# Kernel tuning notes

Measured on AMD Instinct MI355X. Metric: run time of the kernel, lower is better.

Reference implementation:

```python
import jax, jax.numpy as jnp
import numpy as np

TEMPERATURE = 0.07
MARGIN = 0.15
HARD_NEG_RATIO = 0.5


def setup_inputs() -> dict:
    key = jax.random.key(0)
    k1, k2, k3 = jax.random.split(key, 3)
    B, D = 4096, 128
    drug_emb = jax.random.normal(k1, (B, D), dtype=jnp.float32)
    se_emb = jax.random.normal(k2, (B, D), dtype=jnp.float32)
    # labels spread over [0, 5) so that |diff| > 1.0 negatives exist
    labels = jax.random.uniform(k3, (B,), dtype=jnp.float32) * 5.0
    return {"drug_emb": drug_emb, "se_emb": se_emb, "labels": labels}


def _single_branch_loss(z, labels):
    B = z.shape[0]
    # F.normalize(z, dim=-1): divide by norm clamped to eps
    z = z / jnp.maximum(jnp.linalg.norm(z, axis=-1, keepdims=True), 1e-12)
    sim = jnp.matmul(z, z.T) / TEMPERATURE                      # [B, B]
    label_diff = jnp.abs(labels[None, :] - labels[:, None])     # [B, B]
    self_mask = ~jnp.eye(B, dtype=bool)
    pos_weight = jnp.exp(-label_diff / MARGIN) * self_mask      # soft positives
    neg_mask = (label_diff > 1.0) & self_mask

    # k = max(int(mean per-row negative count * ratio), 1), capped at B-1
    mean_negs = jnp.mean(jnp.sum(neg_mask.astype(jnp.float32), axis=1))
    k = jnp.maximum((mean_negs * HARD_NEG_RATIO).astype(jnp.int32), 1)
    k = jnp.minimum(k, B - 1)

    sim_max = jax.lax.stop_gradient(jnp.max(sim, axis=1, keepdims=True))
    logits = sim - sim_max

    # hard-negative top-k per row, as a static-shape rank test (jit-safe)
    neg_sim = jnp.where(neg_mask, sim, -jnp.inf)
    ranks = jnp.argsort(jnp.argsort(-neg_sim, axis=1), axis=1)  # 0 = largest
    hard_neg_mask = (ranks < k) & neg_mask

    any_neg = jnp.any(neg_mask)
    denom_mask = jnp.where(any_neg, hard_neg_mask | (pos_weight > 0.1), self_mask)

    exp_denom = jnp.sum(jnp.exp(logits) * denom_mask, axis=1, keepdims=True) + 1e-8
    log_prob = logits - jnp.log(exp_denom)
    weighted_log_prob = jnp.sum(pos_weight * log_prob, axis=1)
    denom = jnp.maximum(jnp.sum(pos_weight, axis=1), 1e-8)
    return -jnp.mean(weighted_log_prob / denom)


def reference(drug_emb, se_emb, labels):
    loss_drug = _single_branch_loss(drug_emb, labels)
    loss_se = _single_branch_loss(se_emb, labels)
    loss_cross = _single_branch_loss(drug_emb * se_emb, labels)
    return (loss_drug + loss_se + loss_cross) / 3.0
```

## Files before the change

kernel.cpp:

```cpp
#include <hip/hip_runtime.h>
#include <math.h>

#define BB 4096
#define DD 128
#define KLO 0x3E7FFFFFu
#define KHI 0xC1800000u
#define SH0 19
#define NBALLOC 4352

typedef __attribute__((ext_vector_type(8))) short bf16x8;
typedef __attribute__((ext_vector_type(4))) float f32x4;
typedef __attribute__((ext_vector_type(4))) _Float16 f16x4;

__device__ __forceinline__ unsigned fkey(float x){
    int b = __float_as_int(x);
    return (unsigned)(b ^ ((b >> 31) | 0x80000000));
}
__device__ __forceinline__ float funkey(unsigned u){
    unsigned b = (u & 0x80000000u) ? (u & 0x7fffffffu) : ~u;
    return __uint_as_float(b);
}

__device__ __forceinline__ float blkSumF(float v, volatile float* sh){
    #pragma unroll
    for (int o = 32; o > 0; o >>= 1) v += __shfl_down(v, o);
    int t = threadIdx.x;
    __syncthreads();
    if ((t & 63) == 0) sh[t >> 6] = v;
    __syncthreads();
    return (sh[0] + sh[1]) + (sh[2] + sh[3]);
}
__device__ __forceinline__ int blkSumI(int v, volatile int* sh){
    #pragma unroll
    for (int o = 32; o > 0; o >>= 1) v += __shfl_down(v, o);
    int t = threadIdx.x;
    __syncthreads();
    if ((t & 63) == 0) sh[t >> 6] = v;
    __syncthreads();
    return (sh[0] + sh[1]) + (sh[2] + sh[3]);
}

__global__ void krn_normalize(const float* __restrict__ drug, const float* __restrict__ se,
                              ushort* __restrict__ Z){
    int row = blockIdx.x, br = blockIdx.y, t = threadIdx.x;
    float dv = drug[row * DD + t];
    float sv = se[row * DD + t];
    float v = (br == 0) ? dv : ((br == 1) ? sv : dv * sv);
    float sq = v * v;
    #pragma unroll
    for (int o = 32; o > 0; o >>= 1) sq += __shfl_down(sq, o);
    __shared__ float sh[2];
    if ((t & 63) == 0) sh[t >> 6] = sq;
    __syncthreads();
    float nrm = sqrtf(sh[0] + sh[1]);
    float outv = v / fmaxf(nrm, 1e-12f);
    unsigned u = __float_as_uint(outv);
    unsigned r = (u + 0x7FFFu + ((u >> 16) & 1u)) >> 16;
    int col = t ^ ((row & 7) << 3);
    Z[((size_t)br * BB + row) * DD + col] = (ushort)r;
}

__global__ __launch_bounds__(256) void krn_labelstats(const float* __restrict__ labels,
                                                      int* __restrict__ NC,
                                                      float* __restrict__ PWS,
                                                      int* __restrict__ ntot){
    __shared__ float lab[BB];
    __shared__ int shi[4];
    __shared__ float shf[4];
    int t = threadIdx.x;
    #pragma unroll
    for (int e = 0; e < 4; ++e)
        ((float4*)lab)[t + e * 256] = ((const float4*)labels)[t + e * 256];
    __syncthreads();
    int i0 = blockIdx.x * 16;
    int ctot = 0;
    for (int ii = 0; ii < 16; ++ii){
        float li = lab[i0 + ii];
        int c = 0;
        float pws = 0.f;
        #pragma unroll
        for (int e = 0; e < 16; ++e){
            float d = fabsf(li - lab[t + e * 256]);
            c += (d > 1.0f) ? 1 : 0;
            pws += __expf(d * (-1.0f / 0.15f));
        }
        int C = blkSumI(c, shi);
        float P = blkSumF(pws, shf);
        if (t == 0){
            NC[i0 + ii] = C;
            PWS[i0 + ii] = P - 1.0f;
            ctot += C;
        }
    }
    if (t == 0) atomicAdd(ntot, ctot);
}

__global__ void krn_calck(const int* __restrict__ ntot, int* __restrict__ kflags){
    int N = *ntot;
    int k = N >> 13;
    if (k < 1) k = 1;
    if (k > BB - 1) k = BB - 1;
    kflags[0] = k;
    kflags[1] = (N > 0) ? 1 : 0;
}

__device__ __forceinline__ bf16x8 frag_ld(const ushort* base, int row, int e0){
    int e = e0 ^ ((row & 7) << 3);
    return *(const bf16x8*)(base + row * DD + e);
}

__global__ __launch_bounds__(256) void krn_gemm(const ushort* __restrict__ Z,
                                                _Float16* __restrict__ sim, size_t simStride,
                                                int r0){
    __shared__ ushort As[128 * DD];
    __shared__ ushort Bs[128 * DD];
    const ushort* Zb = Z + (size_t)blockIdx.z * (BB * DD);
    _Float16* simz = sim + (size_t)blockIdx.z * simStride;
    int t = threadIdx.x;
    int rowbase = r0 + blockIdx.y * 128;
    int colbase = blockIdx.x * 128;

    {
        const float4* gA = (const float4*)(Zb + (size_t)rowbase * DD);
        const float4* gB = (const float4*)(Zb + (size_t)colbase * DD);
        float4* lA = (float4*)As;
        float4* lB = (float4*)Bs;
        #pragma unroll
        for (int it = 0; it < 8; ++it){
            lA[it * 256 + t] = gA[it * 256 + t];
            lB[it * 256 + t] = gB[it * 256 + t];
        }
    }
    __syncthreads();

    int wid = t >> 6, lane = t & 63;
    int wr = (wid >> 1) * 64, wc = (wid & 1) * 64;
    int fr = lane & 15, fq = lane >> 4;

    f32x4 acc[4][4];
    #pragma unroll
    for (int m = 0; m < 4; ++m)
        #pragma unroll
        for (int n = 0; n < 4; ++n)
            acc[m][n] = (f32x4){0.f, 0.f, 0.f, 0.f};

    #pragma unroll
    for (int ks = 0; ks < 4; ++ks){
        int e0 = ks * 32 + fq * 8;
        bf16x8 a0 = frag_ld(As, wr + 0 * 16 + fr, e0);
        bf16x8 a1 = frag_ld(As, wr + 1 * 16 + fr, e0);
        bf16x8 a2 = frag_ld(As, wr + 2 * 16 + fr, e0);
        bf16x8 a3 = frag_ld(As, wr + 3 * 16 + fr, e0);
        bf16x8 b0 = frag_ld(Bs, wc + 0 * 16 + fr, e0);
        bf16x8 b1 = frag_ld(Bs, wc + 1 * 16 + fr, e0);
        bf16x8 b2 = frag_ld(Bs, wc + 2 * 16 + fr, e0);
        bf16x8 b3 = frag_ld(Bs, wc + 3 * 16 + fr, e0);
        acc[0][0] = __builtin_amdgcn_mfma_f32_16x16x32_bf16(a0, b0, acc[0][0], 0, 0, 0);
        acc[0][1] = __builtin_amdgcn_mfma_f32_16x16x32_bf16(a0, b1, acc[0][1], 0, 0, 0);
        acc[0][2] = __builtin_amdgcn_mfma_f32_16x16x32_bf16(a0, b2, acc[0][2], 0, 0, 0);
        acc[0][3] = __builtin_amdgcn_mfma_f32_16x16x32_bf16(a0, b3, acc[0][3], 0, 0, 0);
        acc[1][0] = __builtin_amdgcn_mfma_f32_16x16x32_bf16(a1, b0, acc[1][0], 0, 0, 0);
        acc[1][1] = __builtin_amdgcn_mfma_f32_16x16x32_bf16(a1, b1, acc[1][1], 0, 0, 0);
        acc[1][2] = __builtin_amdgcn_mfma_f32_16x16x32_bf16(a1, b2, acc[1][2], 0, 0, 0);
        acc[1][3] = __builtin_amdgcn_mfma_f32_16x16x32_bf16(a1, b3, acc[1][3], 0, 0, 0);
        acc[2][0] = __builtin_amdgcn_mfma_f32_16x16x32_bf16(a2, b0, acc[2][0], 0, 0, 0);
        acc[2][1] = __builtin_amdgcn_mfma_f32_16x16x32_bf16(a2, b1, acc[2][1], 0, 0, 0);
        acc[2][2] = __builtin_amdgcn_mfma_f32_16x16x32_bf16(a2, b2, acc[2][2], 0, 0, 0);
        acc[2][3] = __builtin_amdgcn_mfma_f32_16x16x32_bf16(a2, b3, acc[2][3], 0, 0, 0);
        acc[3][0] = __builtin_amdgcn_mfma_f32_16x16x32_bf16(a3, b0, acc[3][0], 0, 0, 0);
        acc[3][1] = __builtin_amdgcn_mfma_f32_16x16x32_bf16(a3, b1, acc[3][1], 0, 0, 0);
        acc[3][2] = __builtin_amdgcn_mfma_f32_16x16x32_bf16(a3, b2, acc[3][2], 0, 0, 0);
        acc[3][3] = __builtin_amdgcn_mfma_f32_16x16x32_bf16(a3, b3, acc[3][3], 0, 0, 0);
    }

    const float invT = 1.0f / 0.07f;
    int srow0 = blockIdx.y * 128 + wr + fq * 4;
    int scol0 = colbase + wc + fr;
    #pragma unroll
    for (int m = 0; m < 4; ++m){
        #pragma unroll
        for (int n = 0; n < 4; ++n){
            f32x4 c = acc[m][n];
            #pragma unroll
            for (int j = 0; j < 4; ++j)
                simz[(size_t)(srow0 + m * 16 + j) * BB + scol0 + n * 16] = (_Float16)(c[j] * invT);
        }
    }
}

__global__ __launch_bounds__(256) void krn_stats(const _Float16* __restrict__ sim, size_t simStride,
                                                 const float* __restrict__ labels,
                                                 const int* __restrict__ NC,
                                                 const float* __restrict__ PWSg,
                                                 const int* __restrict__ kflags,
                                                 float* __restrict__ rowloss, int r0){
    __shared__ int hist[NBALLOC];
    __shared__ int wsum[4];
    __shared__ float redm[4], redb[4];
    __shared__ float redf[4];
    __shared__ unsigned selb[3];
    __shared__ unsigned sel2[2];
    __shared__ int cnt;
    __shared__ unsigned list[96];

    int t = threadIdx.x;
    int bi = blockIdx.y;
    int row = blockIdx.x;
    int i = r0 + row;
    float li = labels[i];

    #pragma unroll
    for (int e = 0; e < 17; ++e) hist[t + e * 256] = 0;
    __syncthreads();

    const _Float16* srow = sim + (size_t)bi * simStride + (size_t)row * BB;
    const f16x4* sp = (const f16x4*)srow;
    const float4* lp = (const float4*)labels;

    float s[16];
    unsigned negbits = 0, posbits = 0;
    float m = -INFINITY, psim = 0.f;

    #pragma unroll
    for (int e = 0; e < 4; ++e){
        f16x4 hv = sp[t + e * 256];
        float4 lv = lp[t + e * 256];
        float lc[4] = {lv.x, lv.y, lv.z, lv.w};
        #pragma unroll
        for (int c = 0; c < 4; ++c){
            int idx = e * 4 + c;
            float v = (float)hv[c];
            s[idx] = v;
            m = fmaxf(m, v);
            float d = fabsf(li - lc[c]);
            float pw = __expf(d * (-1.0f / 0.15f));
            psim = fmaf(pw, v, psim);
            if (d > 1.0f){
                negbits |= 1u << idx;
                atomicAdd(&hist[(fkey(v) - KLO) >> SH0], 1);
            } else if (d < 0.34538776f){
                posbits |= 1u << idx;
            }
        }
    }

    #pragma unroll
    for (int o = 32; o > 0; o >>= 1){
        m = fmaxf(m, __shfl_down(m, o));
        psim += __shfl_down(psim, o);
    }
    __syncthreads();
    if ((t & 63) == 0){
        int w = t >> 6;
        redm[w] = m; redb[w] = psim;
    }
    __syncthreads();
    float M    = fmaxf(fmaxf(redm[0], redm[1]), fmaxf(redm[2], redm[3]));
    float PSIM = (redb[0] + redb[1]) + (redb[2] + redb[3]);

    int kk = kflags[0], anyneg = kflags[1];
    int NCv = NC[i];
    int mode = anyneg ? ((NCv <= kk) ? 1 : 0) : 2;

    unsigned ukth = 0;
    int rfin = 0;
    if (mode == 0){
        unsigned klo = KLO, khi = KHI;
        int sh = SH0;
        int rp = kk;
        bool ready = true;
        while (true){
            if (klo == khi){ ukth = klo; rfin = rp; break; }
            if (!ready){
                #pragma unroll
                for (int e = 0; e < 17; ++e) hist[t + e * 256] = 0;
                __syncthreads();
                #pragma unroll
                for (int idx = 0; idx < 16; ++idx){
                    if (negbits & (1u << idx)){
                        unsigned u = fkey(s[idx]);
                        if (u >= klo && u <= khi)
                            atomicAdd(&hist[(u - klo) >> sh], 1);
                    }
                }
                __syncthreads();
            }
            ready = false;
            int g = 255 - t;
            int base = g * 17;
            int ls = 0;
            #pragma unroll
            for (int e = 0; e < 17; ++e) ls += hist[base + e];
            int v = ls;
            #pragma unroll
            for (int o = 1; o < 64; o <<= 1){
                int u2 = __shfl_up(v, o);
                if ((t & 63) >= o) v += u2;
            }
            if ((t & 63) == 63) wsum[t >> 6] = v;
            __syncthreads();
            int w = t >> 6;
            int pre = (w > 0 ? wsum[0] : 0) + (w > 1 ? wsum[1] : 0) + (w > 2 ? wsum[2] : 0);
            v += pre;
            int aec = v - ls;
            if (aec < rp && rp <= v){
                int cum = aec;
                #pragma unroll
                for (int e = 16; e >= 0; --e){
                    int c = hist[base + e];
                    if (cum < rp && rp <= cum + c){
                        selb[0] = (unsigned)(base + e);
                        selb[1] = (unsigned)cum;
                        selb[2] = (unsigned)c;
                        break;
                    }
                    cum += c;
                }
            }
            __syncthreads();
            unsigned B = selb[0];
            int ae = (int)selb[1];
            int c  = (int)selb[2];
            rp -= ae;
            klo += B << sh;
            unsigned nhi = klo + ((1u << sh) - 1u);
            if (nhi < khi) khi = nhi;
            if (c <= 96){
                if (t == 0) cnt = 0;
                __syncthreads();
                #pragma unroll
                for (int idx = 0; idx < 16; ++idx){
                    if (negbits & (1u << idx)){
                        unsigned u = fkey(s[idx]);
                        if (u >= klo && u <= khi){
                            int p = atomicAdd(&cnt, 1);
                            list[p] = u;
                        }
                    }
                }
                __syncthreads();
                int cc = cnt;
                if (t < cc){
                    unsigned kj = list[t];
                    int g2 = 0, e2 = 0;
                    for (int mm = 0; mm < cc; ++mm){
                        unsigned km = list[mm];
                        g2 += (km > kj) ? 1 : 0;
                        e2 += (km == kj) ? 1 : 0;
                    }
                    if (g2 < rp && rp <= g2 + e2){ sel2[0] = kj; sel2[1] = (unsigned)g2; }
                }
                __syncthreads();
                ukth = sel2[0];
                rfin = rp - (int)sel2[1];
                break;
            }
            {
                unsigned range = khi - klo;
                int bits = 32 - __clz(range);
                sh = (bits > 12) ? (bits - 12) : 0;
            }
            __syncthreads();
        }
    }

    float skth = (mode == 0) ? funkey(ukth) : INFINITY;
    unsigned em = (mode == 2) ? 0xFFFFu : ((mode == 1) ? (negbits | posbits) : posbits);
    float El = 0.f;
    #pragma unroll
    for (int idx = 0; idx < 16; ++idx){
        unsigned bit = 1u << idx;
        bool dm = (em & bit) != 0u;
        if (negbits & bit) dm = dm || (s[idx] > skth);
        if (dm) El += __expf(s[idx] - M);
    }
    float Etot = blkSumF(El, redf);

    if (t == 0){
        if (mode == 0) Etot += (float)rfin * __expf(skth - M);
        float s_self = (float)srow[i];
        Etot -= __expf(s_self - M);
        float PWSc  = PWSg[i];
        float PSIMc = PSIM - s_self;
        float logE = __logf(Etot + 1e-8f);
        float wl = (PSIMc - M * PWSc) - PWSc * logE;
        rowloss[bi * BB + i] = wl / fmaxf(PWSc, 1e-8f);
    }
}

__global__ void krn_final(const float* __restrict__ rowloss, float* __restrict__ out){
    __shared__ float redf[4];
    int t = threadIdx.x;
    float total = 0.f;
    for (int b = 0; b < 3; ++b){
        float ssum = 0.f;
        for (int e = 0; e < 16; ++e) ssum += rowloss[b * BB + t + e * 256];
        float S = blkSumF(ssum, redf);
        total += S * (1.0f / BB);
    }
    if (t == 0) out[0] = -total / 3.0f;
}

extern "C" void kernel_launch(void* const* d_in, const int* in_sizes, int n_in,
                              void* d_out, int out_size, void* d_ws, size_t ws_size,
                              hipStream_t stream){
    const float* drug   = (const float*)d_in[0];
    const float* se     = (const float*)d_in[1];
    const float* labels = (const float*)d_in[2];
    float* out = (float*)d_out;
    char* ws = (char*)d_ws;

    const size_t zbytes = (size_t)3 * BB * DD * sizeof(ushort);
    const size_t tail   = (size_t)(3 + 1 + 1) * BB * sizeof(float) + 256;

    int slab = BB;
    while (slab > 128 && zbytes + tail + (size_t)3 * slab * BB * sizeof(_Float16) > ws_size)
        slab >>= 1;
    size_t simStride = (size_t)slab * BB;

    ushort* Z          = (ushort*)ws;
    _Float16* simbuf   = (_Float16*)(ws + zbytes);
    size_t off         = zbytes + (size_t)3 * simStride * sizeof(_Float16);
    float* rowloss = (float*)(ws + off);  off += (size_t)3 * BB * sizeof(float);
    float* PWSb    = (float*)(ws + off);  off += (size_t)BB * sizeof(float);
    int*   NCb     = (int*)(ws + off);    off += (size_t)BB * sizeof(int);
    int*   ntot    = (int*)(ws + off);
    int*   kflags  = ntot + 2;

    hipMemsetAsync(ntot, 0, 2 * sizeof(int), stream);
    krn_normalize<<<dim3(BB, 3), 128, 0, stream>>>(drug, se, Z);
    krn_labelstats<<<256, 256, 0, stream>>>(labels, NCb, PWSb, ntot);
    krn_calck<<<1, 1, 0, stream>>>(ntot, kflags);

    int nslab = BB / slab;
    for (int s2 = 0; s2 < nslab; ++s2){
        krn_gemm<<<dim3(BB / 128, slab / 128, 3), 256, 0, stream>>>(Z, simbuf, simStride, s2 * slab);
        krn_stats<<<dim3(slab, 3), 256, 0, stream>>>(simbuf, simStride, labels,
                                                     NCb, PWSb, kflags, rowloss, s2 * slab);
    }
    krn_final<<<1, 256, 0, stream>>>(rowloss, out);
}
```

Measured before the change: 191.6 us.

## Store similarity slabs in fp32, cap slab size, shrink histogram bins

The similarity matrix is now written and read as fp32 instead of fp16, and the slab size is capped at 1024 rows, so each slab's buffer (about 48 MB for three branches) is small enough to stay in cache between the GEMM and stats kernels. The radix-select histogram drops from 17 to 9 bins per thread, with the shift widened to match, which cuts LDS clearing and scanning. In exchange, each element moves twice as many bytes, and there are more kernel launches (four slab iterations instead of one).

```diff
diff --git a/kernel.cpp b/kernel.cpp
--- a/kernel.cpp
+++ b/kernel.cpp
@@ -5,12 +5,12 @@
 #define DD 128
 #define KLO 0x3E7FFFFFu
 #define KHI 0xC1800000u
-#define SH0 19
-#define NBALLOC 4352
+#define SH0 20
+#define CHUNK 9
+#define NBALLOC 2304
 
 typedef __attribute__((ext_vector_type(8))) short bf16x8;
 typedef __attribute__((ext_vector_type(4))) float f32x4;
-typedef __attribute__((ext_vector_type(4))) _Float16 f16x4;
 
 __device__ __forceinline__ unsigned fkey(float x){
     int b = __float_as_int(x);
@@ -110,12 +110,12 @@
 }
 
 __global__ __launch_bounds__(256) void krn_gemm(const ushort* __restrict__ Z,
-                                                _Float16* __restrict__ sim, size_t simStride,
+                                                float* __restrict__ sim, size_t simStride,
                                                 int r0){
     __shared__ ushort As[128 * DD];
     __shared__ ushort Bs[128 * DD];
     const ushort* Zb = Z + (size_t)blockIdx.z * (BB * DD);
-    _Float16* simz = sim + (size_t)blockIdx.z * simStride;
+    float* simz = sim + (size_t)blockIdx.z * simStride;
     int t = threadIdx.x;
     int rowbase = r0 + blockIdx.y * 128;
     int colbase = blockIdx.x * 128;
@@ -183,14 +183,14 @@
             f32x4 c = acc[m][n];
             #pragma unroll
             for (int j = 0; j < 4; ++j)
-                simz[(size_t)(srow0 + m * 16 + j) * BB + scol0 + n * 16] = (_Float16)(c[j] * invT);
-        }
-    }
-}
-
-__global__ __launch_bounds__(256) void krn_stats(const _Float16* __restrict__ sim, size_t simStride,
+                simz[(size_t)(srow0 + m * 16 + j) * BB + scol0 + n * 16] = c[j] * invT;
+        }
+    }
+}
+
+__global__ __launch_bounds__(256) void krn_stats(const float* __restrict__ sim, size_t simStride,
                                                  const float* __restrict__ labels,
-                                                 const int* __restrict__ NC,
+                                                 const int* __restrict__ NCg,
                                                  const float* __restrict__ PWSg,
                                                  const int* __restrict__ kflags,
                                                  float* __restrict__ rowloss, int r0){
@@ -210,11 +210,11 @@
     float li = labels[i];
 
     #pragma unroll
-    for (int e = 0; e < 17; ++e) hist[t + e * 256] = 0;
-    __syncthreads();
-
-    const _Float16* srow = sim + (size_t)bi * simStride + (size_t)row * BB;
-    const f16x4* sp = (const f16x4*)srow;
+    for (int e = 0; e < CHUNK; ++e) hist[t + e * 256] = 0;
+    __syncthreads();
+
+    const float* srow = sim + (size_t)bi * simStride + (size_t)row * BB;
+    const float4* sp = (const float4*)srow;
     const float4* lp = (const float4*)labels;
 
     float s[16];
@@ -223,13 +223,14 @@
 
     #pragma unroll
     for (int e = 0; e < 4; ++e){
-        f16x4 hv = sp[t + e * 256];
+        float4 sv = sp[t + e * 256];
         float4 lv = lp[t + e * 256];
+        float sc[4] = {sv.x, sv.y, sv.z, sv.w};
         float lc[4] = {lv.x, lv.y, lv.z, lv.w};
         #pragma unroll
         for (int c = 0; c < 4; ++c){
             int idx = e * 4 + c;
-            float v = (float)hv[c];
+            float v = sc[c];
             s[idx] = v;
             m = fmaxf(m, v);
             float d = fabsf(li - lc[c]);
@@ -259,7 +260,7 @@
     float PSIM = (redb[0] + redb[1]) + (redb[2] + redb[3]);
 
     int kk = kflags[0], anyneg = kflags[1];
-    int NCv = NC[i];
+    int NCv = NCg[i];
     int mode = anyneg ? ((NCv <= kk) ? 1 : 0) : 2;
 
     unsigned ukth = 0;
@@ -273,7 +274,7 @@
             if (klo == khi){ ukth = klo; rfin = rp; break; }
             if (!ready){
                 #pragma unroll
-                for (int e = 0; e < 17; ++e) hist[t + e * 256] = 0;
+                for (int e = 0; e < CHUNK; ++e) hist[t + e * 256] = 0;
                 __syncthreads();
                 #pragma unroll
                 for (int idx = 0; idx < 16; ++idx){
@@ -287,10 +288,10 @@
             }
             ready = false;
             int g = 255 - t;
-            int base = g * 17;
+            int base = g * CHUNK;
             int ls = 0;
             #pragma unroll
-            for (int e = 0; e < 17; ++e) ls += hist[base + e];
+            for (int e = 0; e < CHUNK; ++e) ls += hist[base + e];
             int v = ls;
             #pragma unroll
             for (int o = 1; o < 64; o <<= 1){
@@ -306,7 +307,7 @@
             if (aec < rp && rp <= v){
                 int cum = aec;
                 #pragma unroll
-                for (int e = 16; e >= 0; --e){
+                for (int e = CHUNK - 1; e >= 0; --e){
                     int c = hist[base + e];
                     if (cum < rp && rp <= cum + c){
                         selb[0] = (unsigned)(base + e);
@@ -358,7 +359,7 @@
             {
                 unsigned range = khi - klo;
                 int bits = 32 - __clz(range);
-                sh = (bits > 12) ? (bits - 12) : 0;
+                sh = (bits > 11) ? (bits - 11) : 0;
             }
             __syncthreads();
         }
@@ -378,7 +379,7 @@
 
     if (t == 0){
         if (mode == 0) Etot += (float)rfin * __expf(skth - M);
-        float s_self = (float)srow[i];
+        float s_self = srow[i];
         Etot -= __expf(s_self - M);
         float PWSc  = PWSg[i];
         float PSIMc = PSIM - s_self;
@@ -413,14 +414,14 @@
     const size_t zbytes = (size_t)3 * BB * DD * sizeof(ushort);
     const size_t tail   = (size_t)(3 + 1 + 1) * BB * sizeof(float) + 256;
 
-    int slab = BB;
-    while (slab > 128 && zbytes + tail + (size_t)3 * slab * BB * sizeof(_Float16) > ws_size)
+    int slab = 1024;
+    while (slab > 128 && zbytes + tail + (size_t)3 * slab * BB * sizeof(float) > ws_size)
         slab >>= 1;
     size_t simStride = (size_t)slab * BB;
 
-    ushort* Z          = (ushort*)ws;
-    _Float16* simbuf   = (_Float16*)(ws + zbytes);
-    size_t off         = zbytes + (size_t)3 * simStride * sizeof(_Float16);
+    ushort* Z      = (ushort*)ws;
+    float* simbuf  = (float*)(ws + zbytes);
+    size_t off     = zbytes + (size_t)3 * simStride * sizeof(float);
     float* rowloss = (float*)(ws + off);  off += (size_t)3 * BB * sizeof(float);
     float* PWSb    = (float*)(ws + off);  off += (size_t)BB * sizeof(float);
     int*   NCb     = (int*)(ws + off);    off += (size_t)BB * sizeof(int);
```

After: 240.6 us. 1.26x slower.
